# Kernel tuning notes

Measured on AMD Instinct MI355X. Metric: run time of the kernel, lower is better.

## Reference

```python
import jax, jax.numpy as jnp
import numpy as np

N_EMBD = 768
N_HEAD = 12


def setup_inputs() -> dict:
    key = jax.random.key(0)
    k1, k2, k3, k4, k5 = jax.random.split(key, 5)
    B, T, C = 2, 2048, N_EMBD
    s = 1.0 / np.sqrt(C)
    x = jax.random.normal(k1, (B, T, C), dtype=jnp.float32)
    W_attn = jax.random.uniform(k2, (C, 3 * C), dtype=jnp.float32, minval=-s, maxval=s)
    b_attn = jax.random.uniform(k3, (3 * C,), dtype=jnp.float32, minval=-s, maxval=s)
    W_proj = jax.random.uniform(k4, (C, C), dtype=jnp.float32, minval=-s, maxval=s)
    b_proj = jax.random.uniform(k5, (C,), dtype=jnp.float32, minval=-s, maxval=s)
    return {"x": x, "W_attn": W_attn, "b_attn": b_attn, "W_proj": W_proj, "b_proj": b_proj}


def reference(x, W_attn, b_attn, W_proj, b_proj):
    B, T, C = x.shape
    H = N_HEAD
    D = C // H
    qkv = x @ W_attn + b_attn                      # [B,T,3C]
    q, k, v = jnp.split(qkv, 3, axis=-1)
    q = q.reshape(B, T, H, D).transpose(0, 2, 1, 3)  # [B,H,T,D]
    k = k.reshape(B, T, H, D).transpose(0, 2, 1, 3)
    v = v.reshape(B, T, H, D).transpose(0, 2, 1, 3)
    scale = 1.0 / jnp.sqrt(jnp.asarray(D, dtype=x.dtype))
    scores = jnp.einsum("bhqd,bhkd->bhqk", q, k) * scale  # [B,H,T,T]
    causal = jnp.tril(jnp.ones((T, T), dtype=bool))
    scores = jnp.where(causal, scores, jnp.finfo(x.dtype).min)
    attn = jax.nn.softmax(scores, axis=-1)
    y = jnp.einsum("bhqk,bhkd->bhqd", attn, v)     # [B,H,T,D]
    y = y.transpose(0, 2, 1, 3).reshape(B, T, C)
    return y @ W_proj + b_proj
```

## Files before the change

### kernel.cpp

```cpp
#include <hip/hip_runtime.h>
#include <math.h>

#define N_EMBD 768
#define N_HEAD 12
#define HEAD_DIM 64
#define SEQ 2048
#define BATCH 2

typedef __attribute__((ext_vector_type(8))) short v8s;
typedef __attribute__((ext_vector_type(4))) float v4f;

__device__ __forceinline__ unsigned short f2bf(float f) {
    union { float f; unsigned int u; } x; x.f = f;
    unsigned int u = x.u + 0x7fffu + ((x.u >> 16) & 1u);
    return (unsigned short)(u >> 16);
}
__device__ __forceinline__ float bf2f(unsigned short s) {
    union { unsigned int u; float f; } x; x.u = ((unsigned int)s) << 16;
    return x.f;
}

__device__ __forceinline__ void gload_lds16(const unsigned short* g, unsigned short* l) {
    __builtin_amdgcn_global_load_lds(
        (const __attribute__((address_space(1))) void*)g,
        (__attribute__((address_space(3))) void*)l, 16, 0, 0);
}

#define QSCALE 0.1803368801111396f

__global__ __launch_bounds__(256) void cast_x_kernel(
    const float* __restrict__ in, unsigned short* __restrict__ out)
{
    const int i = (blockIdx.x * 256 + threadIdx.x) * 8;
    const float4 a = *(const float4*)(in + i);
    const float4 b = *(const float4*)(in + i + 4);
    ushort4 s0, s1;
    s0.x = f2bf(a.x); s0.y = f2bf(a.y); s0.z = f2bf(a.z); s0.w = f2bf(a.w);
    s1.x = f2bf(b.x); s1.y = f2bf(b.y); s1.z = f2bf(b.z); s1.w = f2bf(b.w);
    *(ushort4*)(out + i) = s0;
    *(ushort4*)(out + i + 4) = s1;
}

__global__ __launch_bounds__(256) void transpose_cast_kernel(
    const float* __restrict__ in, unsigned short* __restrict__ out, int R, int C)
{
    __shared__ float t[32][33];
    const int bx = blockIdx.x * 32;
    const int by = blockIdx.y * 32;
    const int tx = threadIdx.x & 31, ty = threadIdx.x >> 5;
#pragma unroll
    for (int i = 0; i < 32; i += 8)
        t[ty + i][tx] = in[(size_t)(by + ty + i) * C + bx + tx];
    __syncthreads();
#pragma unroll
    for (int i = 0; i < 32; i += 8)
        out[(size_t)(bx + ty + i) * R + by + tx] = f2bf(t[tx][ty + i]);
}

__global__ __launch_bounds__(256) void qkv_gemm_mfma(
    const unsigned short* __restrict__ A,
    const unsigned short* __restrict__ Bt,
    const float* __restrict__ bias,
    unsigned short* __restrict__ qg,
    unsigned short* __restrict__ kg,
    unsigned short* __restrict__ vg)
{
    __shared__ unsigned short as[128 * 32];
    __shared__ unsigned short bs[128 * 32];
    const int K = 768;
    const int tid = threadIdx.x;
    const int lane = tid & 63;
    const int w = tid >> 6;
    const int wm = w >> 1, wn = w & 1;
    const int quad = lane >> 4, c = lane & 15;
    const int bm = blockIdx.y * 128;
    const int bn = blockIdx.x * 128;

    v4f acc[4][4];
#pragma unroll
    for (int i = 0; i < 4; i++)
#pragma unroll
        for (int j = 0; j < 4; j++) acc[i][j] = (v4f){0.f, 0.f, 0.f, 0.f};

    for (int k0 = 0; k0 < K; k0 += 32) {
        __syncthreads();
#pragma unroll
        for (int p = 0; p < 2; p++) {
            const int idx = p * 256 + tid;
            const int row = idx >> 2;
            const int off = (idx & 3) * 8;
            gload_lds16(A  + (size_t)(bm + row) * K + k0 + off, &as[idx * 8]);
            gload_lds16(Bt + (size_t)(bn + row) * K + k0 + off, &bs[idx * 8]);
        }
        __syncthreads();

        v8s af[4], bf[4];
#pragma unroll
        for (int fm = 0; fm < 4; fm++)
            af[fm] = *(const v8s*)&as[(wm * 64 + fm * 16 + c) * 32 + quad * 8];
#pragma unroll
        for (int fn = 0; fn < 4; fn++)
            bf[fn] = *(const v8s*)&bs[(wn * 64 + fn * 16 + c) * 32 + quad * 8];
#pragma unroll
        for (int fm = 0; fm < 4; fm++)
#pragma unroll
            for (int fn = 0; fn < 4; fn++)
                acc[fm][fn] = __builtin_amdgcn_mfma_f32_16x16x32_bf16(af[fm], bf[fn], acc[fm][fn], 0, 0, 0);
    }

    const int which = bn / N_EMBD;
    const int rem_base = bn - which * N_EMBD;
#pragma unroll
    for (int fm = 0; fm < 4; fm++) {
        const int m0 = bm + wm * 64 + fm * 16 + quad * 4;
        const int b = m0 >> 11;
        const int t0 = m0 & (SEQ - 1);
#pragma unroll
        for (int fn = 0; fn < 4; fn++) {
            const int rem = rem_base + wn * 64 + fn * 16 + c;
            const int h = rem >> 6, d = rem & 63;
            const float bv = bias[bn + wn * 64 + fn * 16 + c];
            const size_t bh = (size_t)(b * N_HEAD + h);
            if (which == 2) {
                ushort4 o;
                o.x = f2bf(acc[fm][fn][0] + bv);
                o.y = f2bf(acc[fm][fn][1] + bv);
                o.z = f2bf(acc[fm][fn][2] + bv);
                o.w = f2bf(acc[fm][fn][3] + bv);
                *(ushort4*)(vg + (bh * 64 + d) * SEQ + t0) = o;
            } else {
                unsigned short* dst = (which == 0) ? qg : kg;
                const float sc = (which == 0) ? QSCALE : 1.0f;
#pragma unroll
                for (int r = 0; r < 4; r++)
                    dst[(bh * SEQ + t0 + r) * 64 + d] = f2bf((acc[fm][fn][r] + bv) * sc);
            }
        }
    }
}

#define PITCH 72

__global__ __launch_bounds__(256) void attn_kernel(
    const unsigned short* __restrict__ qg,
    const unsigned short* __restrict__ kg,
    const unsigned short* __restrict__ vg,
    unsigned short* __restrict__ pO,
    float* __restrict__ pl)
{
    __shared__ unsigned short ks[64 * PITCH];
    __shared__ unsigned short vs[64 * PITCH];
    __shared__ unsigned short ps[4][16 * PITCH];

    const int tid  = threadIdx.x;
    const int w    = tid >> 6;
    const int lane = tid & 63;
    const int quad = lane >> 4;
    const int c    = lane & 15;

    const int bid = (int)blockIdx.x;
    const int bh  = bid % 24;
    const int c2  = 79 - (bid / 24);
    int qt, kc;
    if (c2 < 8)       { qt = c2;                    kc = 0; }
    else if (c2 < 24) { qt = 8 + ((c2 - 8) >> 1);   kc = (c2 - 8) & 1; }
    else if (c2 < 48) { qt = 16 + (c2 - 24) / 3;    kc = (c2 - 24) % 3; }
    else              { qt = 24 + ((c2 - 48) >> 2); kc = (c2 - 48) & 3; }
    const int qbase = qt * 64;

    const unsigned short* qrow = qg + (size_t)bh * SEQ * 64;
    const unsigned short* krow = kg + (size_t)bh * SEQ * 64;
    const unsigned short* vrow = vg + (size_t)bh * 64 * SEQ;

    const unsigned short* qp = qrow + (size_t)(qbase + w * 16 + c) * 64 + quad * 8;
    const v8s bq0 = *(const v8s*)(qp);
    const v8s bq1 = *(const v8s*)(qp + 32);

    v4f oacc[4];
#pragma unroll
    for (int d = 0; d < 4; d++) oacc[d] = (v4f){0.f, 0.f, 0.f, 0.f};
    float l_acc = 0.f;

    const int q_lane = qbase + w * 16 + c;
    unsigned int* psw32 = (unsigned int*)&ps[w][0];

    const int kt0 = kc * 8;
    const int kt1 = min(kt0 + 8, qt + 1);
    for (int kt = kt0; kt < kt1; kt++) {
        const int key0 = kt * 64;
        __syncthreads();
#pragma unroll
        for (int p = 0; p < 2; p++) {
            const int idx = tid + p * 256;
            const int row = idx >> 3, ch = idx & 7;
            uint4 ku = *(const uint4*)(krow + ((size_t)(key0 + row)) * 64 + ch * 8);
            *(uint4*)&ks[row * PITCH + ch * 8] = ku;
            uint4 vu = *(const uint4*)(vrow + (size_t)row * SEQ + key0 + ch * 8);
            *(uint4*)&vs[row * PITCH + ch * 8] = vu;
        }
        __syncthreads();

        v4f sacc[4];
#pragma unroll
        for (int n = 0; n < 4; n++) {
            const v8s ak0 = *(const v8s*)&ks[(n * 16 + c) * PITCH + quad * 8];
            const v8s ak1 = *(const v8s*)&ks[(n * 16 + c) * PITCH + 32 + quad * 8];
            v4f s = (v4f){0.f, 0.f, 0.f, 0.f};
            s = __builtin_amdgcn_mfma_f32_16x16x32_bf16(ak0, bq0, s, 0, 0, 0);
            s = __builtin_amdgcn_mfma_f32_16x16x32_bf16(ak1, bq1, s, 0, 0, 0);
            sacc[n] = s;
        }

        if (kt == qt) {
            const int kb = key0 + quad * 4;
#pragma unroll
            for (int n = 0; n < 4; n++)
#pragma unroll
                for (int r = 0; r < 4; r++)
                    if (kb + n * 16 + r > q_lane) sacc[n][r] = -1e30f;
        }

#pragma unroll
        for (int n = 0; n < 4; n++) {
            float p0 = exp2f(sacc[n][0]);
            float p1 = exp2f(sacc[n][1]);
            float p2 = exp2f(sacc[n][2]);
            float p3 = exp2f(sacc[n][3]);
            l_acc += (p0 + p1) + (p2 + p3);
            const int dw = c * 36 + n * 8 + quad * 2;
            psw32[dw]     = ((unsigned int)f2bf(p1) << 16) | f2bf(p0);
            psw32[dw + 1] = ((unsigned int)f2bf(p3) << 16) | f2bf(p2);
        }

        const v8s ap0 = *(const v8s*)&ps[w][c * PITCH + quad * 8];
        const v8s ap1 = *(const v8s*)&ps[w][c * PITCH + 32 + quad * 8];
#pragma unroll
        for (int d = 0; d < 4; d++) {
            const v8s bv0 = *(const v8s*)&vs[(d * 16 + c) * PITCH + quad * 8];
            const v8s bv1 = *(const v8s*)&vs[(d * 16 + c) * PITCH + 32 + quad * 8];
            oacc[d] = __builtin_amdgcn_mfma_f32_16x16x32_bf16(ap0, bv0, oacc[d], 0, 0, 0);
            oacc[d] = __builtin_amdgcn_mfma_f32_16x16x32_bf16(ap1, bv1, oacc[d], 0, 0, 0);
        }
    }

    l_acc += __shfl_xor(l_acc, 16, 64);
    l_acc += __shfl_xor(l_acc, 32, 64);

    const size_t pidx = (size_t)bh * 80 + c2;
    unsigned short* po = pO + pidx * 4096;
#pragma unroll
    for (int r = 0; r < 4; r++) {
        const int row = w * 16 + quad * 4 + r;
#pragma unroll
        for (int d = 0; d < 4; d++)
            po[row * 64 + d * 16 + c] = f2bf(oacc[d][r]);
    }
    if (lane < 16)
        pl[pidx * 64 + w * 16 + c] = l_acc;
}

__global__ __launch_bounds__(256) void combine_kernel(
    const unsigned short* __restrict__ pO,
    const float* __restrict__ pl,
    unsigned short* __restrict__ y)
{
    const int qt = (int)blockIdx.x;
    const int bh = (int)blockIdx.y;
    int base, nc;
    if (qt < 8)       { base = qt;                 nc = 1; }
    else if (qt < 16) { base = 8 + 2 * (qt - 8);   nc = 2; }
    else if (qt < 24) { base = 24 + 3 * (qt - 16); nc = 3; }
    else              { base = 48 + 4 * (qt - 24); nc = 4; }

    const int row = threadIdx.x >> 2;
    const int colg = (threadIdx.x & 3) * 16;

    float denom = 0.f;
    for (int i = 0; i < nc; i++)
        denom += pl[((size_t)bh * 80 + base + i) * 64 + row];
    const float inv = 1.0f / denom;

    float acc[16];
#pragma unroll
    for (int j = 0; j < 16; j++) acc[j] = 0.f;
    for (int i = 0; i < nc; i++) {
        const unsigned short* po = pO + ((size_t)bh * 80 + base + i) * 4096 + row * 64 + colg;
        ushort4 u0 = *(const ushort4*)(po + 0);
        ushort4 u1 = *(const ushort4*)(po + 4);
        ushort4 u2 = *(const ushort4*)(po + 8);
        ushort4 u3 = *(const ushort4*)(po + 12);
        acc[0]  += bf2f(u0.x); acc[1]  += bf2f(u0.y);
        acc[2]  += bf2f(u0.z); acc[3]  += bf2f(u0.w);
        acc[4]  += bf2f(u1.x); acc[5]  += bf2f(u1.y);
        acc[6]  += bf2f(u1.z); acc[7]  += bf2f(u1.w);
        acc[8]  += bf2f(u2.x); acc[9]  += bf2f(u2.y);
        acc[10] += bf2f(u2.z); acc[11] += bf2f(u2.w);
        acc[12] += bf2f(u3.x); acc[13] += bf2f(u3.y);
        acc[14] += bf2f(u3.z); acc[15] += bf2f(u3.w);
    }

    const int b = bh / N_HEAD;
    const int h = bh - b * N_HEAD;
    const int t = qt * 64 + row;
    unsigned short* yr = y + ((size_t)(b * SEQ + t)) * N_EMBD + h * 64 + colg;
    ushort4 o0, o1, o2, o3;
    o0.x = f2bf(acc[0] * inv);  o0.y = f2bf(acc[1] * inv);
    o0.z = f2bf(acc[2] * inv);  o0.w = f2bf(acc[3] * inv);
    o1.x = f2bf(acc[4] * inv);  o1.y = f2bf(acc[5] * inv);
    o1.z = f2bf(acc[6] * inv);  o1.w = f2bf(acc[7] * inv);
    o2.x = f2bf(acc[8] * inv);  o2.y = f2bf(acc[9] * inv);
    o2.z = f2bf(acc[10] * inv); o2.w = f2bf(acc[11] * inv);
    o3.x = f2bf(acc[12] * inv); o3.y = f2bf(acc[13] * inv);
    o3.z = f2bf(acc[14] * inv); o3.w = f2bf(acc[15] * inv);
    *(ushort4*)(yr + 0)  = o0;
    *(ushort4*)(yr + 4)  = o1;
    *(ushort4*)(yr + 8)  = o2;
    *(ushort4*)(yr + 12) = o3;
}

__global__ __launch_bounds__(256) void proj_gemm_mfma(
    const unsigned short* __restrict__ A,
    const unsigned short* __restrict__ Bt,
    const float* __restrict__ bias,
    float* __restrict__ out)
{
    __shared__ unsigned short as[128 * 32];
    __shared__ unsigned short bs[128 * 32];
    const int K = 768;
    const int tid = threadIdx.x;
    const int lane = tid & 63;
    const int w = tid >> 6;
    const int wm = w >> 1, wn = w & 1;
    const int quad = lane >> 4, c = lane & 15;
    const int bm = blockIdx.y * 128;
    const int bn = blockIdx.x * 128;

    v4f acc[4][4];
#pragma unroll
    for (int i = 0; i < 4; i++)
#pragma unroll
        for (int j = 0; j < 4; j++) acc[i][j] = (v4f){0.f, 0.f, 0.f, 0.f};

    for (int k0 = 0; k0 < K; k0 += 32) {
        __syncthreads();
#pragma unroll
        for (int p = 0; p < 2; p++) {
            const int idx = p * 256 + tid;
            const int row = idx >> 2;
            const int off = (idx & 3) * 8;
            gload_lds16(A  + (size_t)(bm + row) * K + k0 + off, &as[idx * 8]);
            gload_lds16(Bt + (size_t)(bn + row) * K + k0 + off, &bs[idx * 8]);
        }
        __syncthreads();

        v8s af[4], bf[4];
#pragma unroll
        for (int fm = 0; fm < 4; fm++)
            af[fm] = *(const v8s*)&as[(wm * 64 + fm * 16 + c) * 32 + quad * 8];
#pragma unroll
        for (int fn = 0; fn < 4; fn++)
            bf[fn] = *(const v8s*)&bs[(wn * 64 + fn * 16 + c) * 32 + quad * 8];
#pragma unroll
        for (int fm = 0; fm < 4; fm++)
#pragma unroll
            for (int fn = 0; fn < 4; fn++)
                acc[fm][fn] = __builtin_amdgcn_mfma_f32_16x16x32_bf16(af[fm], bf[fn], acc[fm][fn], 0, 0, 0);
    }

#pragma unroll
    for (int fm = 0; fm < 4; fm++) {
        const int m0 = bm + wm * 64 + fm * 16 + quad * 4;
#pragma unroll
        for (int fn = 0; fn < 4; fn++) {
            const int n = bn + wn * 64 + fn * 16 + c;
            const float bv = bias[n];
#pragma unroll
            for (int r = 0; r < 4; r++)
                out[(size_t)(m0 + r) * N_EMBD + n] = acc[fm][fn][r] + bv;
        }
    }
}

extern "C" void kernel_launch(void* const* d_in, const int* in_sizes, int n_in,
                              void* d_out, int out_size, void* d_ws, size_t ws_size,
                              hipStream_t stream) {
    const float* x      = (const float*)d_in[0];
    const float* W_attn = (const float*)d_in[1];
    const float* b_attn = (const float*)d_in[2];
    const float* W_proj = (const float*)d_in[3];
    const float* b_proj = (const float*)d_in[4];
    float* out = (float*)d_out;

    const size_t QSZ = (size_t)BATCH * N_HEAD * SEQ * HEAD_DIM;

    unsigned short* base = (unsigned short*)d_ws;
    unsigned short* xb  = base;
    unsigned short* wta = base + QSZ;
    unsigned short* pO  = base;
    float* pl = (float*)(base + (size_t)1920 * 4096);
    unsigned short* wtp = (unsigned short*)(pl + 1920 * 64);
    unsigned short* qg  = wtp + (size_t)N_EMBD * N_EMBD;
    unsigned short* kg  = qg + QSZ;
    unsigned short* vg  = kg + QSZ;
    unsigned short* yb  = vg + QSZ;

    cast_x_kernel<<<dim3((int)(QSZ / (256 * 8))), 256, 0, stream>>>(x, xb);
    transpose_cast_kernel<<<dim3(72, 24), 256, 0, stream>>>(W_attn, wta, N_EMBD, 3 * N_EMBD);
    transpose_cast_kernel<<<dim3(24, 24), 256, 0, stream>>>(W_proj, wtp, N_EMBD, N_EMBD);

    qkv_gemm_mfma<<<dim3(18, 32), 256, 0, stream>>>(xb, wta, b_attn, qg, kg, vg);
    attn_kernel<<<dim3(80 * 24), 256, 0, stream>>>(qg, kg, vg, pO, pl);
    combine_kernel<<<dim3(32, BATCH * N_HEAD), 256, 0, stream>>>(pO, pl, yb);
    proj_gemm_mfma<<<dim3(6, 32), 256, 0, stream>>>(yb, wtp, b_proj, out);
}
```

Measured before the change: 183.4 us.

## Load K/V tiles via direct global-to-LDS with XOR swizzle instead of padding

Replaces the register-staged K/V tile loads with global_load_lds direct transfers into unpadded LDS tiles. Bank conflicts are avoided with an XOR swizzle on the 16-byte chunk index rather than a row pitch of 72, and the P staging buffer uses the same swizzle. It also packs probabilities to bf16 with a cheaper add-and-permute round instead of full round-to-nearest-even. This removes VGPR round-trips for loads, with slight rounding differences in P and a dependency on the swizzle being consistent across writers and readers.

```diff
diff --git a/kernel.cpp b/kernel.cpp
--- a/kernel.cpp
+++ b/kernel.cpp
@@ -18,6 +18,11 @@
 __device__ __forceinline__ float bf2f(unsigned short s) {
     union { unsigned int u; float f; } x; x.u = ((unsigned int)s) << 16;
     return x.f;
+}
+__device__ __forceinline__ unsigned int pack_bf16(float lo, float hi) {
+    unsigned int ul = __float_as_uint(lo) + 0x8000u;
+    unsigned int uh = __float_as_uint(hi) + 0x8000u;
+    return __builtin_amdgcn_perm(uh, ul, 0x07060302);
 }
 
 __device__ __forceinline__ void gload_lds16(const unsigned short* g, unsigned short* l) {
@@ -139,8 +144,6 @@
     }
 }
 
-#define PITCH 72
-
 __global__ __launch_bounds__(256) void attn_kernel(
     const unsigned short* __restrict__ qg,
     const unsigned short* __restrict__ kg,
@@ -148,9 +151,9 @@
     unsigned short* __restrict__ pO,
     float* __restrict__ pl)
 {
-    __shared__ unsigned short ks[64 * PITCH];
-    __shared__ unsigned short vs[64 * PITCH];
-    __shared__ unsigned short ps[4][16 * PITCH];
+    __shared__ __align__(16) unsigned short ks[64 * 64];
+    __shared__ __align__(16) unsigned short vs[64 * 64];
+    __shared__ __align__(16) unsigned short ps[4][16 * 64];
 
     const int tid  = threadIdx.x;
     const int w    = tid >> 6;
@@ -176,35 +179,40 @@
     const v8s bq0 = *(const v8s*)(qp);
     const v8s bq1 = *(const v8s*)(qp + 32);
 
+    const int r0 = tid >> 3;
+    const int ch0 = (tid & 7) ^ (r0 & 7);
+    const unsigned short* kp0 = krow + (size_t)r0 * 64 + ch0 * 8;
+    const unsigned short* vp0 = vrow + (size_t)r0 * SEQ + ch0 * 8;
+
+    const int swz0 = ((quad ^ (c & 7)) * 8);
+    const int swz1 = swz0 ^ 32;
+
     v4f oacc[4];
 #pragma unroll
     for (int d = 0; d < 4; d++) oacc[d] = (v4f){0.f, 0.f, 0.f, 0.f};
     float l_acc = 0.f;
 
     const int q_lane = qbase + w * 16 + c;
-    unsigned int* psw32 = (unsigned int*)&ps[w][0];
+    unsigned int* pw32 = (unsigned int*)&ps[w][0];
+    const int psq = c & 7;
 
     const int kt0 = kc * 8;
     const int kt1 = min(kt0 + 8, qt + 1);
     for (int kt = kt0; kt < kt1; kt++) {
         const int key0 = kt * 64;
         __syncthreads();
-#pragma unroll
-        for (int p = 0; p < 2; p++) {
-            const int idx = tid + p * 256;
-            const int row = idx >> 3, ch = idx & 7;
-            uint4 ku = *(const uint4*)(krow + ((size_t)(key0 + row)) * 64 + ch * 8);
-            *(uint4*)&ks[row * PITCH + ch * 8] = ku;
-            uint4 vu = *(const uint4*)(vrow + (size_t)row * SEQ + key0 + ch * 8);
-            *(uint4*)&vs[row * PITCH + ch * 8] = vu;
-        }
+        gload_lds16(kp0 + (size_t)key0 * 64, &ks[tid * 8]);
+        gload_lds16(kp0 + (size_t)(key0 + 32) * 64, &ks[(256 + tid) * 8]);
+        gload_lds16(vp0 + key0, &vs[tid * 8]);
+        gload_lds16(vp0 + 32 * SEQ + key0, &vs[(256 + tid) * 8]);
         __syncthreads();
 
         v4f sacc[4];
 #pragma unroll
         for (int n = 0; n < 4; n++) {
-            const v8s ak0 = *(const v8s*)&ks[(n * 16 + c) * PITCH + quad * 8];
-            const v8s ak1 = *(const v8s*)&ks[(n * 16 + c) * PITCH + 32 + quad * 8];
+            const int rb = (n * 16 + c) * 64;
+            const v8s ak0 = *(const v8s*)&ks[rb + swz0];
+            const v8s ak1 = *(const v8s*)&ks[rb + swz1];
             v4f s = (v4f){0.f, 0.f, 0.f, 0.f};
             s = __builtin_amdgcn_mfma_f32_16x16x32_bf16(ak0, bq0, s, 0, 0, 0);
             s = __builtin_amdgcn_mfma_f32_16x16x32_bf16(ak1, bq1, s, 0, 0, 0);
@@ -222,22 +230,24 @@
 
 #pragma unroll
         for (int n = 0; n < 4; n++) {
-            float p0 = exp2f(sacc[n][0]);
-            float p1 = exp2f(sacc[n][1]);
-            float p2 = exp2f(sacc[n][2]);
-            float p3 = exp2f(sacc[n][3]);
+            const float p0 = exp2f(sacc[n][0]);
+            const float p1 = exp2f(sacc[n][1]);
+            const float p2 = exp2f(sacc[n][2]);
+            const float p3 = exp2f(sacc[n][3]);
             l_acc += (p0 + p1) + (p2 + p3);
-            const int dw = c * 36 + n * 8 + quad * 2;
-            psw32[dw]     = ((unsigned int)f2bf(p1) << 16) | f2bf(p0);
-            psw32[dw + 1] = ((unsigned int)f2bf(p3) << 16) | f2bf(p2);
-        }
-
-        const v8s ap0 = *(const v8s*)&ps[w][c * PITCH + quad * 8];
-        const v8s ap1 = *(const v8s*)&ps[w][c * PITCH + 32 + quad * 8];
+            const int sswz = (2 * n + (quad >> 1)) ^ psq;
+            const int dw = c * 32 + sswz * 4 + (quad & 1) * 2;
+            pw32[dw]     = pack_bf16(p0, p1);
+            pw32[dw + 1] = pack_bf16(p2, p3);
+        }
+
+        const v8s ap0 = *(const v8s*)&ps[w][c * 64 + swz0];
+        const v8s ap1 = *(const v8s*)&ps[w][c * 64 + swz1];
 #pragma unroll
         for (int d = 0; d < 4; d++) {
-            const v8s bv0 = *(const v8s*)&vs[(d * 16 + c) * PITCH + quad * 8];
-            const v8s bv1 = *(const v8s*)&vs[(d * 16 + c) * PITCH + 32 + quad * 8];
+            const int rb = (d * 16 + c) * 64;
+            const v8s bv0 = *(const v8s*)&vs[rb + swz0];
+            const v8s bv1 = *(const v8s*)&vs[rb + swz1];
             oacc[d] = __builtin_amdgcn_mfma_f32_16x16x32_bf16(ap0, bv0, oacc[d], 0, 0, 0);
             oacc[d] = __builtin_amdgcn_mfma_f32_16x16x32_bf16(ap1, bv1, oacc[d], 0, 0, 0);
         }
```

Result: faster. 176.5 us (-3.7%).
